# Performance work log

Measured on AMD Instinct MI355X. Metric: run time of the kernel, lower is better.

## Reference

```python
import jax, jax.numpy as jnp
import numpy as np

T, B, INPUT, LATENT = 256, 128, 1024, 2048


def setup_inputs() -> dict:
    key = jax.random.key(0)
    k1, k2, k3, k4, k5 = jax.random.split(key, 5)
    s_i = 1.0 / np.sqrt(INPUT)
    s_h = 1.0 / np.sqrt(LATENT)
    return {
        "x": jax.random.normal(k1, (T, B, INPUT), dtype=jnp.float32),
        "W_i": jax.random.uniform(k2, (LATENT, INPUT), jnp.float32, -s_i, s_i),
        "b_i": jax.random.uniform(k3, (LATENT,), jnp.float32, -s_i, s_i),
        "W_h": jax.random.uniform(k4, (LATENT, LATENT), jnp.float32, -s_h, s_h),
        "b_h": jax.random.uniform(k5, (LATENT,), jnp.float32, -s_h, s_h),
    }


def reference(x, W_i, b_i, W_h, b_h):
    # Precompute the input projection for all timesteps in one big GEMM:
    # [T, B, INPUT] @ [INPUT, LATENT] -> [T, B, LATENT]
    xi = jnp.einsum("tbi,li->tbl", x, W_i) + b_i
    # Step 0: h = None in torch -> tanh(W_i x) only (no W_h term, no b_h).
    h0 = jnp.tanh(xi[0])

    def step(h, xi_t):
        h_new = jnp.tanh(xi_t + h @ W_h.T + b_h)
        return h_new, h_new

    _, hs = jax.lax.scan(step, h0, xi[1:])
    # [T, B, LATENT]
    return jnp.concatenate([h0[None], hs], axis=0)
```

## Files before the change

### kernel.cpp

```cpp
#include <hip/hip_runtime.h>
#include <hip/hip_bf16.h>
#include <math.h>

#define T_STEPS 256
#define BATCH   128
#define IN_DIM  1024
#define LAT     2048
#define NBLK    256

#define NG      8
#define GB      32
#define GROWS   16
#define GCOLS   64

typedef __bf16 bf16x8 __attribute__((ext_vector_type(8)));
typedef __bf16 bf16x4 __attribute__((ext_vector_type(4)));
typedef float  f32x4  __attribute__((ext_vector_type(4)));
typedef float  f32x2  __attribute__((ext_vector_type(2)));

#define MFMA16 __builtin_amdgcn_mfma_f32_16x16x32_bf16

__device__ __forceinline__ unsigned int poll_sc1(const unsigned int* p) {
    unsigned int v;
    asm volatile("global_load_dword %0, %1, off sc1" : "=v"(v) : "v"(p) : "memory");
    asm volatile("s_waitcnt vmcnt(0)" ::: "memory");
    return v;
}
__device__ __forceinline__ void st_sc1(unsigned int* p, unsigned int v) {
    asm volatile("global_store_dword %0, %1, off sc1" :: "v"(p), "v"(v) : "memory");
}
__device__ __forceinline__ unsigned int pack_bf16(float a, float b) {
    union { __bf16 h[2]; unsigned int u; } p;
    p.h[0] = (__bf16)a; p.h[1] = (__bf16)b;
    return p.u;
}

__device__ __forceinline__ int swz(int row, int kbyte) {
    return (row * 64 + kbyte) ^ ((row & 7) << 4);
}

template<int ROWS>
__device__ __forceinline__ void stage_load(const float* __restrict__ src, int ld,
                                           int tid, f32x4* regs) {
#pragma unroll
    for (int rnd = 0; rnd < ROWS / 32; ++rnd) {
        int r  = rnd * 32 + (tid >> 3);
        int kc = (tid & 7) * 4;
        regs[rnd] = *(const f32x4*)(src + (size_t)r * ld + kc);
    }
}

template<int ROWS>
__device__ __forceinline__ void stage_write(const f32x4* regs, char* hi, char* lo,
                                            int tid) {
#pragma unroll
    for (int rnd = 0; rnd < ROWS / 32; ++rnd) {
        int r  = rnd * 32 + (tid >> 3);
        int kc = (tid & 7) * 4;
        bf16x4 vh, vl;
        f32x4  v = regs[rnd];
#pragma unroll
        for (int e = 0; e < 4; ++e) {
            float x = v[e];
            __bf16 h = (__bf16)x;
            vh[e] = h;
            vl[e] = (__bf16)(x - (float)h);
        }
        int off = swz(r, kc * 2);
        *(bf16x4*)(hi + off) = vh;
        *(bf16x4*)(lo + off) = vl;
    }
}

__device__ __forceinline__ bf16x8 ld_frag(const char* p, int row, int kb) {
    return *(const bf16x8*)(p + swz(row, kb));
}

__device__ __forceinline__ void split8(f32x4 v0, f32x4 v1, bf16x8& hi, bf16x8& lo) {
#pragma unroll
    for (int e = 0; e < 4; ++e) {
        __bf16 h0 = (__bf16)v0[e];
        hi[e]     = h0;
        lo[e]     = (__bf16)(v0[e] - (float)h0);
        __bf16 h1 = (__bf16)v1[e];
        hi[e + 4] = h1;
        lo[e + 4] = (__bf16)(v1[e] - (float)h1);
    }
}

__global__ __launch_bounds__(256)
void k_prep(const float* __restrict__ W, __bf16* __restrict__ hi)
{
    size_t i = ((size_t)blockIdx.x * 256 + threadIdx.x) * 4;
    f32x4 v = *(const f32x4*)(W + i);
    bf16x4 vh;
#pragma unroll
    for (int e = 0; e < 4; ++e) vh[e] = (__bf16)v[e];
    *(bf16x4*)(hi + i) = vh;
}

__global__ __launch_bounds__(256, 2)
void k_xproj(const float* __restrict__ x, const float* __restrict__ Wi,
             const float* __restrict__ bi, float* __restrict__ out,
             __bf16* __restrict__ h0hi)
{
    __shared__ __align__(16) char lds[32 * 1024];
    char* Ahi = lds;
    char* Alo = lds + 8192;
    char* Bhi = lds + 16384;
    char* Blo = lds + 24576;

    int tid  = threadIdx.x;
    int lane = tid & 63;
    int w    = tid >> 6;
    int wm   = (w >> 1) * 64;
    int wn   = (w & 1) * 64;
    int bm   = blockIdx.y * 128;
    int bn   = blockIdx.x * 128;

    const float* Abase = x  + (size_t)bm * IN_DIM;
    const float* Bbase = Wi + (size_t)bn * IN_DIM;

    f32x4 acc[4][4] = {};
    f32x4 ra[4], rb[4];

    stage_load<128>(Abase, IN_DIM, tid, ra);
    stage_load<128>(Bbase, IN_DIM, tid, rb);

    for (int k0 = 0; k0 < IN_DIM; k0 += 32) {
        stage_write<128>(ra, Ahi, Alo, tid);
        stage_write<128>(rb, Bhi, Blo, tid);
        __syncthreads();

        if (k0 + 32 < IN_DIM) {
            stage_load<128>(Abase + k0 + 32, IN_DIM, tid, ra);
            stage_load<128>(Bbase + k0 + 32, IN_DIM, tid, rb);
        }

        int kb = (lane >> 4) * 16;
        bf16x8 ah[4], al[4], bh[4], bl[4];
#pragma unroll
        for (int i = 0; i < 4; ++i) {
            int rrow = i * 16 + (lane & 15);
            ah[i] = ld_frag(Ahi, wm + rrow, kb);
            al[i] = ld_frag(Alo, wm + rrow, kb);
            bh[i] = ld_frag(Bhi, wn + rrow, kb);
            bl[i] = ld_frag(Blo, wn + rrow, kb);
        }
#pragma unroll
        for (int i = 0; i < 4; ++i)
#pragma unroll
            for (int j = 0; j < 4; ++j) {
                acc[i][j] = MFMA16(ah[i], bh[j], acc[i][j], 0, 0, 0);
                acc[i][j] = MFMA16(ah[i], bl[j], acc[i][j], 0, 0, 0);
                acc[i][j] = MFMA16(al[i], bh[j], acc[i][j], 0, 0, 0);
            }
        __syncthreads();
    }

#pragma unroll
    for (int j = 0; j < 4; ++j) {
        int n = bn + wn + j * 16 + (lane & 15);
        float bias = bi[n];
#pragma unroll
        for (int i = 0; i < 4; ++i) {
            int m0 = bm + wm + i * 16 + ((lane >> 4) * 4);
#pragma unroll
            for (int r = 0; r < 4; ++r) {
                float v = acc[i][j][r] + bias;
                if (m0 + r < BATCH) {
                    v = tanhf(v);
                    if (h0hi)
                        h0hi[(size_t)(m0 + r) * LAT + n] = (__bf16)v;
                }
                out[(size_t)(m0 + r) * LAT + n] = v;
            }
        }
    }
}

#define LOADA_S(dst, base, off)                                               \
    asm volatile("global_load_dwordx4 %0, %1, off offset:" #off " sc1"        \
                 : "=v"(dst) : "v"(base) : "memory")

#define LOADB(dst, base, off)                                                 \
    asm volatile("global_load_dwordx4 %0, %1, off offset:" #off               \
                 : "=v"(dst) : "v"(base))

template<bool FRESH>
__device__ __forceinline__ void recur_body(
    const __bf16* __restrict__ Whi, __bf16* __restrict__ hpl,
    const float* __restrict__ bias, float* __restrict__ out,
    unsigned int* __restrict__ flags,
    float (&part)[8][GROWS][GCOLS + 2],
    int tid, int lane, int w, int rg, int cb, int bm, int bn)
{
    const int fr    = lane & 15;
    const int kq    = (lane >> 4) * 8;
    const int kbase = w * 256 + kq;
    const size_t HN = (size_t)BATCH * LAT;

    bf16x8 bq[4][8];
    {
        const __bf16* B0 = Whi + (size_t)(bn + fr) * LAT + kbase;
        const __bf16* B1 = B0 + (size_t)16 * LAT;
        const __bf16* B2 = B0 + (size_t)32 * LAT;
        const __bf16* B3 = B0 + (size_t)48 * LAT;
        LOADB(bq[0][0], B0,   0); LOADB(bq[0][1], B0,  64);
        LOADB(bq[0][2], B0, 128); LOADB(bq[0][3], B0, 192);
        LOADB(bq[0][4], B0, 256); LOADB(bq[0][5], B0, 320);
        LOADB(bq[0][6], B0, 384); LOADB(bq[0][7], B0, 448);
        LOADB(bq[1][0], B1,   0); LOADB(bq[1][1], B1,  64);
        LOADB(bq[1][2], B1, 128); LOADB(bq[1][3], B1, 192);
        LOADB(bq[1][4], B1, 256); LOADB(bq[1][5], B1, 320);
        LOADB(bq[1][6], B1, 384); LOADB(bq[1][7], B1, 448);
        LOADB(bq[2][0], B2,   0); LOADB(bq[2][1], B2,  64);
        LOADB(bq[2][2], B2, 128); LOADB(bq[2][3], B2, 192);
        LOADB(bq[2][4], B2, 256); LOADB(bq[2][5], B2, 320);
        LOADB(bq[2][6], B2, 384); LOADB(bq[2][7], B2, 448);
        LOADB(bq[3][0], B3,   0); LOADB(bq[3][1], B3,  64);
        LOADB(bq[3][2], B3, 128); LOADB(bq[3][3], B3, 192);
        LOADB(bq[3][4], B3, 256); LOADB(bq[3][5], B3, 320);
        LOADB(bq[3][6], B3, 384); LOADB(bq[3][7], B3, 448);
        asm volatile("s_waitcnt vmcnt(0)" ::: "memory");
        __builtin_amdgcn_sched_barrier(0);
    }

    const int    orow = tid >> 5;
    const int    oc   = (tid & 31) * 2;
    const size_t idx  = (size_t)(bm + orow) * LAT + bn + oc;
    const float  bv0  = bias[bn + oc];
    const float  bv1  = bias[bn + oc + 1];

    f32x2 xv = *(const f32x2*)(out + (size_t)1 * (BATCH * LAT) + idx);

    for (int t = 1; t < T_STEPS; ++t) {
        float* io = out + (size_t)t * (BATCH * LAT);

        if (t > 1) {
            const unsigned int* fp =
                flags + ((size_t)(t - 1) * NG + rg) * GB + w * 4;
            for (;;) {
                unsigned int f = 1;
                if (lane < 4) f = poll_sc1(fp + lane);
                if (__all(f != 0)) break;
                __builtin_amdgcn_s_sleep(1);
            }
        }

        const __bf16* Aplane = FRESH ? hpl + HN * (size_t)(t - 1)
                                     : hpl + HN * (size_t)((t - 1) & 1);
        const __bf16* Ar = Aplane + (size_t)(bm + fr) * LAT + kbase;

        bf16x8 a[8];
        if constexpr (FRESH) {
#pragma unroll
            for (int i = 0; i < 8; ++i)
                a[i] = *(const bf16x8*)(Ar + i * 32);
        } else {
            LOADA_S(a[0], Ar,   0); LOADA_S(a[1], Ar,  64);
            LOADA_S(a[2], Ar, 128); LOADA_S(a[3], Ar, 192);
            LOADA_S(a[4], Ar, 256); LOADA_S(a[5], Ar, 320);
            LOADA_S(a[6], Ar, 384); LOADA_S(a[7], Ar, 448);
            asm volatile("s_waitcnt vmcnt(0)" ::: "memory");
            __builtin_amdgcn_sched_barrier(0);
        }

        f32x4 acc[4] = {};
#pragma unroll
        for (int i = 0; i < 8; ++i)
#pragma unroll
            for (int cf = 0; cf < 4; ++cf)
                acc[cf] = MFMA16(a[i], bq[cf][i], acc[cf], 0, 0, 0);

        f32x2 xn = {};
        if (t + 1 < T_STEPS)
            xn = *(const f32x2*)(out + (size_t)(t + 1) * (BATCH * LAT) + idx);

#pragma unroll
        for (int cf = 0; cf < 4; ++cf)
#pragma unroll
            for (int r = 0; r < 4; ++r)
                part[w][(lane >> 4) * 4 + r][cf * 16 + fr] = acc[cf][r];

        __syncthreads();

        float s0 = 0.f, s1 = 0.f;
#pragma unroll
        for (int p = 0; p < 8; ++p) {
            f32x2 v = *(const f32x2*)&part[p][orow][oc];
            s0 += v[0];
            s1 += v[1];
        }

        float o0 = tanhf(s0 + bv0 + xv[0]);
        float o1 = tanhf(s1 + bv1 + xv[1]);

        __bf16* Np = FRESH ? hpl + HN * (size_t)t
                           : hpl + HN * (size_t)(t & 1);
        st_sc1((unsigned int*)(Np + idx), pack_bf16(o0, o1));

        asm volatile("s_waitcnt vmcnt(0)" ::: "memory");
        __syncthreads();
        if (tid == 0 && t + 1 < T_STEPS)
            st_sc1(flags + ((size_t)t * NG + rg) * GB + cb, 1u);

        f32x2 ov; ov[0] = o0; ov[1] = o1;
        *(f32x2*)(io + idx) = ov;

        xv = xn;
    }
}

template<bool FRESH>
__global__ __launch_bounds__(512, 2)
void k_recur(const __bf16* __restrict__ Whi, __bf16* __restrict__ hpl,
             const float* __restrict__ bias, float* __restrict__ out,
             unsigned int* __restrict__ flags)
{
    __shared__ __align__(16) float part[8][GROWS][GCOLS + 2];

    const int tid  = threadIdx.x;
    const int lane = tid & 63;
    const int w    = tid >> 6;

    const int bid = blockIdx.x;
    const int rg  = bid & 7;
    const int cb  = bid >> 3;
    const int bm  = rg * GROWS;
    const int bn  = cb * GCOLS;

    recur_body<FRESH>(Whi, hpl, bias, out, flags, part,
                      tid, lane, w, rg, cb, bm, bn);
}

__global__ __launch_bounds__(256, 2)
void k_step_f32(const float* __restrict__ hprev, const float* __restrict__ Wh,
                const float* __restrict__ bias, float* __restrict__ io)
{
    __shared__ __align__(16) float part[4][32][32];

    const int tid  = threadIdx.x;
    const int lane = tid & 63;
    const int w    = tid >> 6;

    const int id  = blockIdx.x;
    const int j_  = id >> 3;
    const int bn  = ((id & 7) * 8 + (j_ >> 2)) * 32;
    const int bm  = (j_ & 3) * 32;

    const int fr = lane & 15;
    const int kq = (lane >> 4) * 8;

    const float* A0 = hprev + (size_t)(bm + fr)      * LAT;
    const float* A1 = hprev + (size_t)(bm + 16 + fr) * LAT;
    const float* B0 = Wh    + (size_t)(bn + fr)      * LAT;
    const float* B1 = Wh    + (size_t)(bn + 16 + fr) * LAT;

    f32x4 acc[2][2] = {};
    const int kbase = w * 512 + kq;
#pragma unroll
    for (int i = 0; i < 16; ++i) {
        const int k = kbase + i * 32;
        f32x4 a00 = *(const f32x4*)(A0 + k);
        f32x4 a01 = *(const f32x4*)(A0 + k + 4);
        f32x4 a10 = *(const f32x4*)(A1 + k);
        f32x4 a11 = *(const f32x4*)(A1 + k + 4);
        f32x4 b00 = *(const f32x4*)(B0 + k);
        f32x4 b01 = *(const f32x4*)(B0 + k + 4);
        f32x4 b10 = *(const f32x4*)(B1 + k);
        f32x4 b11 = *(const f32x4*)(B1 + k + 4);

        bf16x8 ah0, al0, ah1, al1, bh0, bl0, bh1, bl1;
        split8(a00, a01, ah0, al0);
        split8(a10, a11, ah1, al1);
        split8(b00, b01, bh0, bl0);
        split8(b10, b11, bh1, bl1);

        acc[0][0] = MFMA16(ah0, bh0, acc[0][0], 0, 0, 0);
        acc[0][1] = MFMA16(ah0, bh1, acc[0][1], 0, 0, 0);
        acc[1][0] = MFMA16(ah1, bh0, acc[1][0], 0, 0, 0);
        acc[1][1] = MFMA16(ah1, bh1, acc[1][1], 0, 0, 0);
        acc[0][0] = MFMA16(al0, bh0, acc[0][0], 0, 0, 0);
        acc[0][1] = MFMA16(al0, bh1, acc[0][1], 0, 0, 0);
        acc[1][0] = MFMA16(al1, bh0, acc[1][0], 0, 0, 0);
        acc[1][1] = MFMA16(al1, bh1, acc[1][1], 0, 0, 0);
        acc[0][0] = MFMA16(ah0, bl0, acc[0][0], 0, 0, 0);
        acc[0][1] = MFMA16(ah0, bl1, acc[0][1], 0, 0, 0);
        acc[1][0] = MFMA16(ah1, bl0, acc[1][0], 0, 0, 0);
        acc[1][1] = MFMA16(ah1, bl1, acc[1][1], 0, 0, 0);
    }

#pragma unroll
    for (int mi = 0; mi < 2; ++mi)
#pragma unroll
        for (int nj = 0; nj < 2; ++nj)
#pragma unroll
            for (int r = 0; r < 4; ++r)
                part[w][mi * 16 + (lane >> 4) * 4 + r][nj * 16 + fr] = acc[mi][nj][r];

    __syncthreads();

    const int row = tid >> 3;
    const int c   = (tid & 7) * 4;
    f32x4 s0 = *(const f32x4*)&part[0][row][c];
    f32x4 s1 = *(const f32x4*)&part[1][row][c];
    f32x4 s2 = *(const f32x4*)&part[2][row][c];
    f32x4 s3 = *(const f32x4*)&part[3][row][c];

    float* outp = io + (size_t)(bm + row) * LAT + bn + c;
    f32x4 xv = *(const f32x4*)outp;
    f32x4 bv = *(const f32x4*)(bias + bn + c);
    f32x4 o;
#pragma unroll
    for (int e = 0; e < 4; ++e)
        o[e] = tanhf(s0[e] + s1[e] + s2[e] + s3[e] + xv[e] + bv[e]);
    *(f32x4*)outp = o;
}

extern "C" void kernel_launch(void* const* d_in, const int* in_sizes, int n_in,
                              void* d_out, int out_size, void* d_ws, size_t ws_size,
                              hipStream_t stream) {
    const float* x  = (const float*)d_in[0];
    const float* Wi = (const float*)d_in[1];
    const float* bi = (const float*)d_in[2];
    const float* Wh = (const float*)d_in[3];
    const float* bh = (const float*)d_in[4];
    float* out = (float*)d_out;

    const size_t whbytes = (size_t)LAT * LAT * 2;
    const size_t hbytes  = (size_t)BATCH * LAT * 2;
    const size_t fbytes  = (size_t)T_STEPS * NG * GB * sizeof(unsigned int);

    const size_t need_fresh = whbytes + (size_t)T_STEPS * hbytes + fbytes;
    const size_t need_pp    = whbytes + 2 * hbytes + fbytes;

    const bool fresh = ws_size >= need_fresh;
    const bool pp    = !fresh && ws_size >= need_pp;

    char* wsb = (char*)d_ws;
    __bf16* Whi = (__bf16*)wsb;
    __bf16* hpl = (__bf16*)(wsb + whbytes);
    const size_t nplanes = fresh ? T_STEPS : 2;
    unsigned int* flags = (unsigned int*)(wsb + whbytes + nplanes * hbytes);

    if (fresh || pp) {
        hipMemsetAsync(flags, 0, fbytes, stream);
        k_prep<<<(LAT * LAT) / (256 * 4), 256, 0, stream>>>(Wh, Whi);
    }

    dim3 g1(LAT / 128, (T_STEPS * BATCH) / 128);
    k_xproj<<<g1, 256, 0, stream>>>(x, Wi, bi, out,
                                    (fresh || pp) ? hpl : nullptr);

    if (fresh) {
        k_recur<true ><<<NBLK, 512, 0, stream>>>(Whi, hpl, bh, out, flags);
    } else if (pp) {
        k_recur<false><<<NBLK, 512, 0, stream>>>(Whi, hpl, bh, out, flags);
    } else {
        for (int t = 1; t < T_STEPS; ++t)
            k_step_f32<<<256, 256, 0, stream>>>(out + (size_t)(t - 1) * BATCH * LAT,
                                                Wh, bh,
                                                out + (size_t)t * BATCH * LAT);
    }
}
```

Baseline: 1.420 ms.

## Use bitmask atomic flags and coalesced LDS-staged h stores in recurrence

Per-step completion flags shrink from one word per column block to a single 32-bit bitmask per row group, set with an atomic OR. Each wave now polls one word for its 4 required bits instead of 4 lanes polling separate words with sleeps. The new hidden state is staged through shared memory so 128 threads write 16-byte coalesced stores instead of 512 threads writing 4-byte stores. The next-step x prefetch moves after the store, and the change adds an extra barrier plus atomic contention on one word per group.

```diff
diff --git a/kernel.cpp b/kernel.cpp
--- a/kernel.cpp
+++ b/kernel.cpp
@@ -17,6 +17,7 @@
 typedef __bf16 bf16x4 __attribute__((ext_vector_type(4)));
 typedef float  f32x4  __attribute__((ext_vector_type(4)));
 typedef float  f32x2  __attribute__((ext_vector_type(2)));
+typedef unsigned int u32x4 __attribute__((ext_vector_type(4)));
 
 #define MFMA16 __builtin_amdgcn_mfma_f32_16x16x32_bf16
 
@@ -25,9 +26,6 @@
     asm volatile("global_load_dword %0, %1, off sc1" : "=v"(v) : "v"(p) : "memory");
     asm volatile("s_waitcnt vmcnt(0)" ::: "memory");
     return v;
-}
-__device__ __forceinline__ void st_sc1(unsigned int* p, unsigned int v) {
-    asm volatile("global_store_dword %0, %1, off sc1" :: "v"(p), "v"(v) : "memory");
 }
 __device__ __forceinline__ unsigned int pack_bf16(float a, float b) {
     union { __bf16 h[2]; unsigned int u; } p;
@@ -193,6 +191,7 @@
     const float* __restrict__ bias, float* __restrict__ out,
     unsigned int* __restrict__ flags,
     float (&part)[8][GROWS][GCOLS + 2],
+    unsigned int (&stg)[GROWS][36],
     int tid, int lane, int w, int rg, int cb, int bm, int bn)
 {
     const int fr    = lane & 15;
@@ -232,20 +231,16 @@
     const float  bv0  = bias[bn + oc];
     const float  bv1  = bias[bn + oc + 1];
 
-    f32x2 xv = *(const f32x2*)(out + (size_t)1 * (BATCH * LAT) + idx);
+    const unsigned int need = 0xFu << (w * 4);
+
+    f32x2 xv = *(const f32x2*)(out + (size_t)1 * HN + idx);
 
     for (int t = 1; t < T_STEPS; ++t) {
-        float* io = out + (size_t)t * (BATCH * LAT);
+        float* io = out + (size_t)t * HN;
 
         if (t > 1) {
-            const unsigned int* fp =
-                flags + ((size_t)(t - 1) * NG + rg) * GB + w * 4;
-            for (;;) {
-                unsigned int f = 1;
-                if (lane < 4) f = poll_sc1(fp + lane);
-                if (__all(f != 0)) break;
-                __builtin_amdgcn_s_sleep(1);
-            }
+            const unsigned int* fp = flags + (size_t)(t - 1) * NG + rg;
+            while ((poll_sc1(fp) & need) != need) { }
         }
 
         const __bf16* Aplane = FRESH ? hpl + HN * (size_t)(t - 1)
@@ -273,10 +268,6 @@
             for (int cf = 0; cf < 4; ++cf)
                 acc[cf] = MFMA16(a[i], bq[cf][i], acc[cf], 0, 0, 0);
 
-        f32x2 xn = {};
-        if (t + 1 < T_STEPS)
-            xn = *(const f32x2*)(out + (size_t)(t + 1) * (BATCH * LAT) + idx);
-
 #pragma unroll
         for (int cf = 0; cf < 4; ++cf)
 #pragma unroll
@@ -296,19 +287,29 @@
         float o0 = tanhf(s0 + bv0 + xv[0]);
         float o1 = tanhf(s1 + bv1 + xv[1]);
 
+        stg[orow][tid & 31] = pack_bf16(o0, o1);
+        __syncthreads();
+
         __bf16* Np = FRESH ? hpl + HN * (size_t)t
                            : hpl + HN * (size_t)(t & 1);
-        st_sc1((unsigned int*)(Np + idx), pack_bf16(o0, o1));
-
-        asm volatile("s_waitcnt vmcnt(0)" ::: "memory");
+        if (tid < 128) {
+            int row = tid >> 3, seg = tid & 7;
+            u32x4 val = *(const u32x4*)&stg[row][seg * 4];
+            __bf16* dst = Np + (size_t)(bm + row) * LAT + bn + seg * 8;
+            asm volatile("global_store_dwordx4 %0, %1, off sc1"
+                         :: "v"(dst), "v"(val) : "memory");
+            asm volatile("s_waitcnt vmcnt(0)" ::: "memory");
+        }
         __syncthreads();
+
         if (tid == 0 && t + 1 < T_STEPS)
-            st_sc1(flags + ((size_t)t * NG + rg) * GB + cb, 1u);
+            __hip_atomic_fetch_or(flags + (size_t)t * NG + rg, 1u << cb,
+                                  __ATOMIC_RELAXED, __HIP_MEMORY_SCOPE_AGENT);
 
         f32x2 ov; ov[0] = o0; ov[1] = o1;
         *(f32x2*)(io + idx) = ov;
-
-        xv = xn;
+        if (t + 1 < T_STEPS)
+            xv = *(const f32x2*)(out + (size_t)(t + 1) * HN + idx);
     }
 }
 
@@ -319,6 +320,7 @@
              unsigned int* __restrict__ flags)
 {
     __shared__ __align__(16) float part[8][GROWS][GCOLS + 2];
+    __shared__ __align__(16) unsigned int stg[GROWS][36];
 
     const int tid  = threadIdx.x;
     const int lane = tid & 63;
@@ -330,7 +332,7 @@
     const int bm  = rg * GROWS;
     const int bn  = cb * GCOLS;
 
-    recur_body<FRESH>(Whi, hpl, bias, out, flags, part,
+    recur_body<FRESH>(Whi, hpl, bias, out, flags, part, stg,
                       tid, lane, w, rg, cb, bm, bn);
 }
 
@@ -430,7 +432,7 @@
 
     const size_t whbytes = (size_t)LAT * LAT * 2;
     const size_t hbytes  = (size_t)BATCH * LAT * 2;
-    const size_t fbytes  = (size_t)T_STEPS * NG * GB * sizeof(unsigned int);
+    const size_t fbytes  = (size_t)T_STEPS * NG * sizeof(unsigned int);
 
     const size_t need_fresh = whbytes + (size_t)T_STEPS * hbytes + fbytes;
     const size_t need_pp    = whbytes + 2 * hbytes + fbytes;
```

Measured after the change: 1.512 ms. 1.06x slower.
